# Performance work log

Hardware: AMD Instinct MI355X
Metric: run time of the kernel (lower is better)

## Reference

```python
import jax, jax.numpy as jnp
import numpy as np

N_INTT = 100000
N_MVTX = 100000
N_EDGES = 300000
IN_DIM = 64
OUT_DIM = 64
FEAT_DIM = 2 * OUT_DIM          # 128
EDGE_DIM = 2 * FEAT_DIM         # 256
H_DIM = IN_DIM + FEAT_DIM + 2 * EDGE_DIM  # 64+128+512 = 704


def _lin(key, fan_in, fan_out):
    k1, k2 = jax.random.split(key)
    bound = 1.0 / np.sqrt(fan_in)
    W = jax.random.uniform(k1, (fan_in, fan_out), jnp.float32, -bound, bound)
    b = jax.random.uniform(k2, (fan_out,), jnp.float32, -bound, bound)
    return W, b


def setup_inputs() -> dict:
    key = jax.random.key(0)
    ks = jax.random.split(key, 12)
    x_intt_0 = jax.random.normal(ks[0], (N_INTT, 3), jnp.float32)
    x_mvtx_0 = jax.random.normal(ks[1], (N_MVTX, 3), jnp.float32)
    x_intt = jax.random.normal(ks[2], (N_INTT, IN_DIM), jnp.float32)
    x_mvtx = jax.random.normal(ks[3], (N_MVTX, IN_DIM), jnp.float32)
    start = jax.random.randint(ks[4], (N_EDGES,), 0, N_INTT, jnp.int32)
    end = jax.random.randint(ks[5], (N_EDGES,), 0, N_MVTX, jnp.int32)
    edge_index = jnp.stack([start, end], axis=0)
    W_in_intt, b_in_intt = _lin(ks[6], IN_DIM, FEAT_DIM)
    W_in_mvtx, b_in_mvtx = _lin(ks[7], IN_DIM, FEAT_DIM)
    W_score, b_score = _lin(ks[8], EDGE_DIM, 1)
    W_out_intt, b_out_intt = _lin(ks[9], H_DIM, OUT_DIM)
    W_out_mvtx, b_out_mvtx = _lin(ks[10], H_DIM, OUT_DIM)
    return {
        "x_intt_0": x_intt_0, "x_mvtx_0": x_mvtx_0,
        "x_intt": x_intt, "x_mvtx": x_mvtx, "edge_index": edge_index,
        "W_in_intt": W_in_intt, "b_in_intt": b_in_intt,
        "W_in_mvtx": W_in_mvtx, "b_in_mvtx": b_in_mvtx,
        "W_score": W_score, "b_score": b_score,
        "W_out_intt": W_out_intt, "b_out_intt": b_out_intt,
        "W_out_mvtx": W_out_mvtx, "b_out_mvtx": b_out_mvtx,
    }


def _mean_max_pool(edges, idx, num_segments):
    # scatter_mean with zero-initialized out: mean over incident edges, 0 if none
    s = jax.ops.segment_sum(edges, idx, num_segments=num_segments)
    cnt = jax.ops.segment_sum(jnp.ones((edges.shape[0], 1), edges.dtype), idx,
                              num_segments=num_segments)
    mean = s / jnp.maximum(cnt, 1.0)
    # scatter_max with zero-initialized out: max includes the initial 0
    mx = jnp.maximum(jax.ops.segment_max(edges, idx, num_segments=num_segments), 0.0)
    return mean, mx


def reference(x_intt_0, x_mvtx_0, x_intt, x_mvtx, edge_index,
              W_in_intt, b_in_intt, W_in_mvtx, b_in_mvtx,
              W_score, b_score, W_out_intt, b_out_intt,
              W_out_mvtx, b_out_mvtx):
    # apply_constraints=False -> x_intt_0/x_mvtx_0 unused
    xp_intt = x_intt @ W_in_intt + b_in_intt        # [Ni, F]
    xp_mvtx = x_mvtx @ W_in_mvtx + b_in_mvtx        # [Nm, F]
    start, end = edge_index[0], edge_index[1]
    xp = jnp.concatenate([xp_intt[start], xp_mvtx[end]], axis=-1)  # [E, 2F]
    att = jnp.exp(-jnp.abs(xp @ W_score + b_score))  # potential activation, [E,1]
    edges = xp * att                                 # [E, 2F]
    mean_i, max_i = _mean_max_pool(edges, start, xp_intt.shape[0])
    mean_m, max_m = _mean_max_pool(edges, end, xp_mvtx.shape[0])
    H_intt = jnp.concatenate([x_intt, xp_intt, mean_i, max_i], axis=-1)  # [Ni, 704]
    H_mvtx = jnp.concatenate([x_mvtx, xp_mvtx, mean_m, max_m], axis=-1)
    h_intt = jax.nn.relu(H_intt @ W_out_intt + b_out_intt)
    h_mvtx = jax.nn.relu(H_mvtx @ W_out_mvtx + b_out_mvtx)
    return (h_intt, h_mvtx)
```

## Files before the change

### kernel.cpp

```cpp
#include <hip/hip_runtime.h>
#include <hip/hip_bf16.h>

typedef __hip_bfloat16 bf16;
typedef __attribute__((ext_vector_type(8))) short bf16x8;
typedef __attribute__((ext_vector_type(4))) float f32x4;

__device__ __forceinline__ float bfu(unsigned u) { return __uint_as_float(u << 16); }
__device__ __forceinline__ unsigned packbf(float a, float b) {
    return (unsigned)__bfloat16_as_ushort(__float2bfloat16(a)) |
           ((unsigned)__bfloat16_as_ushort(__float2bfloat16(b)) << 16);
}

#define CAP 32

#define NEL_O (704 * 64)

__global__ __launch_bounds__(256) void prep_kernel(
    const int* __restrict__ e_start, const int* __restrict__ e_end,
    int* __restrict__ deg_i, int* __restrict__ deg_m,
    int* __restrict__ list_i, int* __restrict__ list_m, int E, int fill_blocks,
    const float* __restrict__ Woi, const float* __restrict__ Wom,
    bf16* __restrict__ Wtoi, bf16* __restrict__ Wtom,
    const float* __restrict__ Wii, const float* __restrict__ Wim, int wt_blocks,
    const float* __restrict__ x_i, const float* __restrict__ b_i,
    const float* __restrict__ x_m, const float* __restrict__ b_m,
    const float* __restrict__ Wsc,
    bf16* __restrict__ xp_i, bf16* __restrict__ xp_m,
    float* __restrict__ sc_i, float* __restrict__ sc_m,
    int Ni, int Nm, int lin_bi)
{
    int bid = blockIdx.x;
    if (bid < fill_blocks) {
        int i = bid * 256 + threadIdx.x;
        if (i >= E) return;
        int s = e_start[i], e = e_end[i];
        int pi = atomicAdd(&deg_i[s], 1);
        if (pi < CAP) list_i[(size_t)s * CAP + pi] = e;
        int pm = atomicAdd(&deg_m[e], 1);
        if (pm < CAP) list_m[(size_t)e * CAP + pm] = s;
        return;
    }
    bid -= fill_blocks;
    if (bid < wt_blocks) {
        int tid = bid * 256 + threadIdx.x;
        if (tid >= 2 * NEL_O) return;
        int half = tid >= NEL_O;
        int t = tid - half * NEL_O;
        int j = t / 704, k = t % 704;
        const float* W = half ? Wom : Woi;
        bf16* Wt = half ? Wtom : Wtoi;
        Wt[(size_t)j * 704 + k] = __float2bfloat16(W[(size_t)k * 64 + j]);
        return;
    }
    bid -= wt_blocks;
    int side = bid >= lin_bi;
    int blk = side ? bid - lin_bi : bid;
    const float* x   = side ? x_m : x_i;
    const float* Win = side ? Wim : Wii;
    const float* b   = side ? b_m : b_i;
    const float* wsc = side ? Wsc + 128 : Wsc;
    bf16* xp = side ? xp_m : xp_i;
    float* sc = side ? sc_m : sc_i;
    int N = side ? Nm : Ni;

    int tid = threadIdx.x, wv = tid >> 6, lane = tid & 63;
    int frow = lane & 15, kg = lane >> 4;
    int n0 = blk * 64 + wv * 16;
    if (n0 >= N) return;
    int nrow = min(n0 + frow, N - 1);
    f32x4 acc[8];
#pragma unroll
    for (int nt = 0; nt < 8; ++nt) acc[nt] = (f32x4){0.f, 0.f, 0.f, 0.f};
#pragma unroll
    for (int kk = 0; kk < 2; ++kk) {
        const float* ap = x + (size_t)nrow * 64 + kk * 32 + kg * 8;
        float4 a0 = *(const float4*)ap;
        float4 a1 = *(const float4*)(ap + 4);
        union { unsigned u[4]; bf16x8 v; } au;
        au.u[0] = packbf(a0.x, a0.y); au.u[1] = packbf(a0.z, a0.w);
        au.u[2] = packbf(a1.x, a1.y); au.u[3] = packbf(a1.z, a1.w);
#pragma unroll
        for (int nt = 0; nt < 8; ++nt) {
            int col = nt * 16 + frow;
            const float* wp = Win + (size_t)(kk * 32 + kg * 8) * 128 + col;
            union { unsigned u[4]; bf16x8 v; } bu;
#pragma unroll
            for (int z = 0; z < 4; ++z)
                bu.u[z] = packbf(wp[(2 * z) * 128], wp[(2 * z + 1) * 128]);
            acc[nt] = __builtin_amdgcn_mfma_f32_16x16x32_bf16(au.v, bu.v, acc[nt], 0, 0, 0);
        }
    }
    float contrib[4] = {0.f, 0.f, 0.f, 0.f};
#pragma unroll
    for (int nt = 0; nt < 8; ++nt) {
        int col = nt * 16 + frow;
        float bj = b[col];
        float wj = wsc[col];
#pragma unroll
        for (int reg = 0; reg < 4; ++reg) {
            float v = acc[nt][reg] + bj;
            int n = n0 + kg * 4 + reg;
            if (n < N) xp[(size_t)n * 128 + col] = __float2bfloat16(v);
            contrib[reg] += v * wj;
        }
    }
#pragma unroll
    for (int off = 1; off < 16; off <<= 1) {
#pragma unroll
        for (int reg = 0; reg < 4; ++reg)
            contrib[reg] += __shfl_xor(contrib[reg], off, 64);
    }
    if (frow == 0) {
#pragma unroll
        for (int reg = 0; reg < 4; ++reg) {
            int n = n0 + kg * 4 + reg;
            if (n < N) sc[n] = contrib[reg];
        }
    }
}

#define BN 16
#define HS 716
__device__ __forceinline__ void accum8(uint4 g, float att, float* s, float* m) {
    unsigned gg[4] = {g.x, g.y, g.z, g.w};
#pragma unroll
    for (int k = 0; k < 4; ++k) {
        float t0 = att * bfu(gg[k] & 0xffffu);
        float t1 = att * bfu(gg[k] >> 16);
        s[2 * k] += t0;  s[2 * k + 1] += t1;
        m[2 * k] = fmaxf(m[2 * k], t0);  m[2 * k + 1] = fmaxf(m[2 * k + 1], t1);
    }
}

__global__ __launch_bounds__(256) void node_kernel(
    const float* __restrict__ x_i, const bf16* __restrict__ xp_i,
    const bf16* __restrict__ xp_m,
    const float* __restrict__ sc_i, const float* __restrict__ sc_m,
    const int* __restrict__ deg_i, const int* __restrict__ list_i,
    const bf16* __restrict__ Wt_oi, const float* __restrict__ b_oi,
    const float* __restrict__ x_m,
    const int* __restrict__ deg_m, const int* __restrict__ list_m,
    const bf16* __restrict__ Wt_om, const float* __restrict__ b_om,
    const float* __restrict__ bsc, float* __restrict__ out,
    int Ni, int Nm, int blocks_i)
{
    __shared__ bf16 Hs[BN][HS];
    int side = (int)blockIdx.x >= blocks_i;
    int blk = side ? blockIdx.x - blocks_i : blockIdx.x;
    const float* x        = side ? x_m : x_i;
    const bf16* xp_self   = side ? xp_m : xp_i;
    const bf16* xp_other  = side ? xp_i : xp_m;
    const float* sc_self  = side ? sc_m : sc_i;
    const float* sc_other = side ? sc_i : sc_m;
    const int* deg  = side ? deg_m : deg_i;
    const int* list = side ? list_m : list_i;
    const bf16* Wt  = side ? Wt_om : Wt_oi;
    const float* b  = side ? b_om : b_oi;
    float* outp = side ? out + (size_t)Ni * 64 : out;
    int N = side ? Nm : Ni;
    int self_first = side ? 0 : 1;

    int tid = threadIdx.x, wv = tid >> 6, lane = tid & 63;
    int ql = lane & 15, q4 = lane & 48;
    int r = wv * 4 + (lane >> 4);
    int n0 = blk * BN;
    int n = min(n0 + r, N - 1);

    float bias = bsc[0];
    int dg = deg[n];
    int dgc = min(dg, CAP);
    float ps = sc_self[n] + bias;
    uint4 us4 = *(const uint4*)(xp_self + (size_t)n * 128 + ql * 8);
    float4 xv4 = *(const float4*)(x + (size_t)n * 64 + ql * 4);

    int oa = 0, ob = 0;
    float sa = 0.f, sb = 0.f;
    if (ql < dgc)      oa = list[(size_t)n * CAP + ql];
    if (16 + ql < dgc) ob = list[(size_t)n * CAP + 16 + ql];
    if (ql < dgc)      sa = sc_other[oa];
    if (16 + ql < dgc) sb = sc_other[ob];
    float att_a = (ql < dgc)      ? __expf(-fabsf(ps + sa)) : 0.f;
    float att_b = (16 + ql < dgc) ? __expf(-fabsf(ps + sb)) : 0.f;

    float A = att_a + att_b;
    float Am = fmaxf(att_a, att_b);
#pragma unroll
    for (int off = 1; off < 16; off <<= 1) {
        A += __shfl_xor(A, off, 64);
        Am = fmaxf(Am, __shfl_xor(Am, off, 64));
    }

    float s[8], m[8];
#pragma unroll
    for (int k = 0; k < 8; ++k) { s[k] = 0.f; m[k] = 0.f; }

    int dmaxw = dgc;
    dmaxw = max(dmaxw, __shfl_xor(dmaxw, 16, 64));
    dmaxw = max(dmaxw, __shfl_xor(dmaxw, 32, 64));

    int dm0 = min(dmaxw, 16);
    for (int d = 0; d < dm0; d += 4) {
        uint4 g[4];
        float a[4];
#pragma unroll
        for (int j = 0; j < 4; ++j) {
            int dd = min(d + j, 15);
            bool p = (d + j < dgc);
            int o = __shfl(oa, q4 + dd, 64);
            a[j] = p ? __shfl(att_a, q4 + dd, 64) : 0.f;
            g[j] = (uint4){0u, 0u, 0u, 0u};
            if (p) g[j] = *(const uint4*)(xp_other + (size_t)o * 128 + ql * 8);
        }
#pragma unroll
        for (int j = 0; j < 4; ++j) accum8(g[j], a[j], s, m);
    }
    for (int d = 16; d < dmaxw; d += 2) {
#pragma unroll
        for (int j = 0; j < 2; ++j) {
            int dd = min(d + j - 16, 15);
            bool p = (d + j < dgc);
            int o = __shfl(ob, q4 + dd, 64);
            float a0 = p ? __shfl(att_b, q4 + dd, 64) : 0.f;
            uint4 g0 = (uint4){0u, 0u, 0u, 0u};
            if (p) g0 = *(const uint4*)(xp_other + (size_t)o * 128 + ql * 8);
            accum8(g0, a0, s, m);
        }
    }

    float inv = 1.0f / fmaxf((float)dg, 1.0f);
    float sA = A * inv, sAm = Am;
    int cm_self  = self_first ? 192 : 320;
    int cm_cross = self_first ? 320 : 192;
    int cx_self  = self_first ? 448 : 576;
    int cx_cross = self_first ? 576 : 448;
    char* row = (char*)&Hs[r][0];
    *(uint2*)(row + ql * 8) = make_uint2(packbf(xv4.x, xv4.y), packbf(xv4.z, xv4.w));
    *(uint4*)(row + 128 + ql * 16) = us4;
    unsigned uu[4] = {us4.x, us4.y, us4.z, us4.w};
    float xs[8];
#pragma unroll
    for (int k = 0; k < 4; ++k) {
        xs[2 * k] = bfu(uu[k] & 0xffffu);
        xs[2 * k + 1] = bfu(uu[k] >> 16);
    }
    uint4 wms, wxs, wmc, wxc;
    wms.x = packbf(xs[0] * sA, xs[1] * sA);  wms.y = packbf(xs[2] * sA, xs[3] * sA);
    wms.z = packbf(xs[4] * sA, xs[5] * sA);  wms.w = packbf(xs[6] * sA, xs[7] * sA);
    wxs.x = packbf(fmaxf(xs[0], 0.f) * sAm, fmaxf(xs[1], 0.f) * sAm);
    wxs.y = packbf(fmaxf(xs[2], 0.f) * sAm, fmaxf(xs[3], 0.f) * sAm);
    wxs.z = packbf(fmaxf(xs[4], 0.f) * sAm, fmaxf(xs[5], 0.f) * sAm);
    wxs.w = packbf(fmaxf(xs[6], 0.f) * sAm, fmaxf(xs[7], 0.f) * sAm);
    wmc.x = packbf(s[0] * inv, s[1] * inv);  wmc.y = packbf(s[2] * inv, s[3] * inv);
    wmc.z = packbf(s[4] * inv, s[5] * inv);  wmc.w = packbf(s[6] * inv, s[7] * inv);
    wxc.x = packbf(m[0], m[1]);  wxc.y = packbf(m[2], m[3]);
    wxc.z = packbf(m[4], m[5]);  wxc.w = packbf(m[6], m[7]);
    *(uint4*)(row + cm_self * 2 + ql * 16)  = wms;
    *(uint4*)(row + cx_self * 2 + ql * 16)  = wxs;
    *(uint4*)(row + cm_cross * 2 + ql * 16) = wmc;
    *(uint4*)(row + cx_cross * 2 + ql * 16) = wxc;
    __syncthreads();

    int frow = lane & 15;
    int kg = lane >> 4;
    const char* abase = (const char*)&Hs[frow][0] + kg * 16;
    const char* bbase = (const char*)(Wt + (size_t)(wv * 16 + frow) * 704) + kg * 16;
    f32x4 acc = {0.f, 0.f, 0.f, 0.f};
#pragma unroll
    for (int kt = 0; kt < 22; ++kt) {
        bf16x8 a  = *(const bf16x8*)(abase + kt * 64);
        bf16x8 bf = *(const bf16x8*)(bbase + kt * 64);
        acc = __builtin_amdgcn_mfma_f32_16x16x32_bf16(a, bf, acc, 0, 0, 0);
    }
    int ccol = wv * 16 + frow;
    float bj = b[ccol];
#pragma unroll
    for (int reg = 0; reg < 4; ++reg) {
        int crow = kg * 4 + reg;
        int nn = n0 + crow;
        if (nn < N) outp[(size_t)nn * 64 + ccol] = fmaxf(acc[reg] + bj, 0.f);
    }
}

extern "C" void kernel_launch(void* const* d_in, const int* in_sizes, int n_in,
                              void* d_out, int out_size, void* d_ws, size_t ws_size,
                              hipStream_t stream) {
    const float* x_i    = (const float*)d_in[2];
    const float* x_m    = (const float*)d_in[3];
    const int*   eidx   = (const int*)d_in[4];
    const float* W_in_i = (const float*)d_in[5];
    const float* b_in_i = (const float*)d_in[6];
    const float* W_in_m = (const float*)d_in[7];
    const float* b_in_m = (const float*)d_in[8];
    const float* W_sc   = (const float*)d_in[9];
    const float* b_sc   = (const float*)d_in[10];
    const float* W_o_i  = (const float*)d_in[11];
    const float* b_o_i  = (const float*)d_in[12];
    const float* W_o_m  = (const float*)d_in[13];
    const float* b_o_m  = (const float*)d_in[14];

    int Ni = in_sizes[2] / 64;
    int Nm = in_sizes[3] / 64;
    int E  = in_sizes[4] / 2;
    const int* e_start = eidx;
    const int* e_end   = eidx + E;

    char* base = (char*)d_ws;
    bf16* xp_i  = (bf16*)base;  base += (size_t)Ni * 128 * sizeof(bf16);
    bf16* xp_m  = (bf16*)base;  base += (size_t)Nm * 128 * sizeof(bf16);
    float* sc_i = (float*)base; base += (size_t)Ni * sizeof(float);
    float* sc_m = (float*)base; base += (size_t)Nm * sizeof(float);
    int* list_i = (int*)base;   base += (size_t)Ni * CAP * sizeof(int);
    int* list_m = (int*)base;   base += (size_t)Nm * CAP * sizeof(int);
    int* deg_i  = (int*)base;   base += (size_t)Ni * sizeof(int);
    int* deg_m  = (int*)base;   base += (size_t)Nm * sizeof(int);
    bf16* Wt_oi = (bf16*)base;  base += (size_t)704 * 64 * sizeof(bf16);
    bf16* Wt_om = (bf16*)base;  base += (size_t)704 * 64 * sizeof(bf16);
    hipMemsetAsync(deg_i, 0, ((size_t)Ni + Nm) * sizeof(int), stream);

    int fill_blocks = (E + 255) / 256;
    int wt_blocks = (2 * NEL_O + 255) / 256;
    int lin_bi = (Ni + 63) / 64, lin_bm = (Nm + 63) / 64;
    prep_kernel<<<fill_blocks + wt_blocks + lin_bi + lin_bm, 256, 0, stream>>>(
        e_start, e_end, deg_i, deg_m, list_i, list_m, E, fill_blocks,
        W_o_i, W_o_m, Wt_oi, Wt_om, W_in_i, W_in_m, wt_blocks,
        x_i, b_in_i, x_m, b_in_m, W_sc,
        xp_i, xp_m, sc_i, sc_m, Ni, Nm, lin_bi);

    float* out = (float*)d_out;
    int nb_i = (Ni + BN - 1) / BN, nb_m = (Nm + BN - 1) / BN;
    node_kernel<<<nb_i + nb_m, 256, 0, stream>>>(
        x_i, xp_i, xp_m, sc_i, sc_m, deg_i, list_i, Wt_oi, b_o_i,
        x_m, deg_m, list_m, Wt_om, b_o_m, b_sc, out, Ni, Nm, nb_i);
}
```

Baseline: 221.7 us.

## Precompute edge attention in separate fill kernel and store bf16 copies of x

Moves adjacency-list construction into its own kernel that runs after the projection kernel. It computes each edge's attention weight once and stores it next to the neighbor index as a uint2 pair. The node kernel no longer gathers score values per neighbor or evaluates exp. Node features are also cached as bf16 during the projection stage so the node kernel reads half the bytes, and output stores are made nontemporal. In exchange it adds a kernel launch, serializes the fill step after the projection, and doubles the size of the adjacency lists.

Measured after the change: 230.7 us. 1.04x slower.

```diff
diff --git a/kernel.cpp b/kernel.cpp
--- a/kernel.cpp
+++ b/kernel.cpp
@@ -4,6 +4,7 @@
 typedef __hip_bfloat16 bf16;
 typedef __attribute__((ext_vector_type(8))) short bf16x8;
 typedef __attribute__((ext_vector_type(4))) float f32x4;
+typedef __attribute__((ext_vector_type(2))) unsigned u32x2;
 
 __device__ __forceinline__ float bfu(unsigned u) { return __uint_as_float(u << 16); }
 __device__ __forceinline__ unsigned packbf(float a, float b) {
@@ -12,13 +13,9 @@
 }
 
 #define CAP 32
-
 #define NEL_O (704 * 64)
 
 __global__ __launch_bounds__(256) void prep_kernel(
-    const int* __restrict__ e_start, const int* __restrict__ e_end,
-    int* __restrict__ deg_i, int* __restrict__ deg_m,
-    int* __restrict__ list_i, int* __restrict__ list_m, int E, int fill_blocks,
     const float* __restrict__ Woi, const float* __restrict__ Wom,
     bf16* __restrict__ Wtoi, bf16* __restrict__ Wtom,
     const float* __restrict__ Wii, const float* __restrict__ Wim, int wt_blocks,
@@ -26,21 +23,11 @@
     const float* __restrict__ x_m, const float* __restrict__ b_m,
     const float* __restrict__ Wsc,
     bf16* __restrict__ xp_i, bf16* __restrict__ xp_m,
+    bf16* __restrict__ xb_i, bf16* __restrict__ xb_m,
     float* __restrict__ sc_i, float* __restrict__ sc_m,
     int Ni, int Nm, int lin_bi)
 {
     int bid = blockIdx.x;
-    if (bid < fill_blocks) {
-        int i = bid * 256 + threadIdx.x;
-        if (i >= E) return;
-        int s = e_start[i], e = e_end[i];
-        int pi = atomicAdd(&deg_i[s], 1);
-        if (pi < CAP) list_i[(size_t)s * CAP + pi] = e;
-        int pm = atomicAdd(&deg_m[e], 1);
-        if (pm < CAP) list_m[(size_t)e * CAP + pm] = s;
-        return;
-    }
-    bid -= fill_blocks;
     if (bid < wt_blocks) {
         int tid = bid * 256 + threadIdx.x;
         if (tid >= 2 * NEL_O) return;
@@ -60,6 +47,7 @@
     const float* b   = side ? b_m : b_i;
     const float* wsc = side ? Wsc + 128 : Wsc;
     bf16* xp = side ? xp_m : xp_i;
+    bf16* xb = side ? xb_m : xb_i;
     float* sc = side ? sc_m : sc_i;
     int N = side ? Nm : Ni;
 
@@ -79,6 +67,7 @@
         union { unsigned u[4]; bf16x8 v; } au;
         au.u[0] = packbf(a0.x, a0.y); au.u[1] = packbf(a0.z, a0.w);
         au.u[2] = packbf(a1.x, a1.y); au.u[3] = packbf(a1.z, a1.w);
+        *(bf16x8*)(xb + (size_t)nrow * 64 + kk * 32 + kg * 8) = au.v;
 #pragma unroll
         for (int nt = 0; nt < 8; ++nt) {
             int col = nt * 16 + frow;
@@ -119,6 +108,24 @@
     }
 }
 
+__global__ __launch_bounds__(256) void fill_kernel(
+    const int* __restrict__ e_start, const int* __restrict__ e_end,
+    const float* __restrict__ sc_i, const float* __restrict__ sc_m,
+    const float* __restrict__ bsc,
+    int* __restrict__ deg_i, int* __restrict__ deg_m,
+    uint2* __restrict__ list_i, uint2* __restrict__ list_m, int E)
+{
+    int i = blockIdx.x * 256 + threadIdx.x;
+    if (i >= E) return;
+    int s = e_start[i], e = e_end[i];
+    float att = __expf(-fabsf(sc_i[s] + sc_m[e] + bsc[0]));
+    unsigned au = __float_as_uint(att);
+    int pi = atomicAdd(&deg_i[s], 1);
+    if (pi < CAP) list_i[(size_t)s * CAP + pi] = make_uint2((unsigned)e, au);
+    int pm = atomicAdd(&deg_m[e], 1);
+    if (pm < CAP) list_m[(size_t)e * CAP + pm] = make_uint2((unsigned)s, au);
+}
+
 #define BN 16
 #define HS 716
 __device__ __forceinline__ void accum8(uint4 g, float att, float* s, float* m) {
@@ -133,27 +140,23 @@
 }
 
 __global__ __launch_bounds__(256) void node_kernel(
-    const float* __restrict__ x_i, const bf16* __restrict__ xp_i,
+    const bf16* __restrict__ xb_i, const bf16* __restrict__ xp_i,
     const bf16* __restrict__ xp_m,
-    const float* __restrict__ sc_i, const float* __restrict__ sc_m,
-    const int* __restrict__ deg_i, const int* __restrict__ list_i,
+    const int* __restrict__ deg_i, const uint2* __restrict__ list_i,
     const bf16* __restrict__ Wt_oi, const float* __restrict__ b_oi,
-    const float* __restrict__ x_m,
-    const int* __restrict__ deg_m, const int* __restrict__ list_m,
+    const bf16* __restrict__ xb_m,
+    const int* __restrict__ deg_m, const uint2* __restrict__ list_m,
     const bf16* __restrict__ Wt_om, const float* __restrict__ b_om,
-    const float* __restrict__ bsc, float* __restrict__ out,
-    int Ni, int Nm, int blocks_i)
+    float* __restrict__ out, int Ni, int Nm, int blocks_i)
 {
     __shared__ bf16 Hs[BN][HS];
     int side = (int)blockIdx.x >= blocks_i;
     int blk = side ? blockIdx.x - blocks_i : blockIdx.x;
-    const float* x        = side ? x_m : x_i;
+    const bf16* xb        = side ? xb_m : xb_i;
     const bf16* xp_self   = side ? xp_m : xp_i;
     const bf16* xp_other  = side ? xp_i : xp_m;
-    const float* sc_self  = side ? sc_m : sc_i;
-    const float* sc_other = side ? sc_i : sc_m;
     const int* deg  = side ? deg_m : deg_i;
-    const int* list = side ? list_m : list_i;
+    const uint2* list = side ? list_m : list_i;
     const bf16* Wt  = side ? Wt_om : Wt_oi;
     const float* b  = side ? b_om : b_oi;
     float* outp = side ? out + (size_t)Ni * 64 : out;
@@ -166,21 +169,16 @@
     int n0 = blk * BN;
     int n = min(n0 + r, N - 1);
 
-    float bias = bsc[0];
     int dg = deg[n];
     int dgc = min(dg, CAP);
-    float ps = sc_self[n] + bias;
     uint4 us4 = *(const uint4*)(xp_self + (size_t)n * 128 + ql * 8);
-    float4 xv4 = *(const float4*)(x + (size_t)n * 64 + ql * 4);
-
-    int oa = 0, ob = 0;
-    float sa = 0.f, sb = 0.f;
-    if (ql < dgc)      oa = list[(size_t)n * CAP + ql];
-    if (16 + ql < dgc) ob = list[(size_t)n * CAP + 16 + ql];
-    if (ql < dgc)      sa = sc_other[oa];
-    if (16 + ql < dgc) sb = sc_other[ob];
-    float att_a = (ql < dgc)      ? __expf(-fabsf(ps + sa)) : 0.f;
-    float att_b = (16 + ql < dgc) ? __expf(-fabsf(ps + sb)) : 0.f;
+    u32x2 xv = *(const u32x2*)(xb + (size_t)n * 64 + ql * 4);
+
+    int d16 = min(dgc, 16);
+    uint2 ea = (ql < d16)       ? list[(size_t)n * CAP + ql]      : make_uint2(0u, 0u);
+    uint2 eb = (16 + ql < dgc)  ? list[(size_t)n * CAP + 16 + ql] : make_uint2(0u, 0u);
+    int oa = (int)ea.x;  float att_a = __uint_as_float(ea.y);
+    int ob = (int)eb.x;  float att_b = __uint_as_float(eb.y);
 
     float A = att_a + att_b;
     float Am = fmaxf(att_a, att_b);
@@ -234,7 +232,7 @@
     int cx_self  = self_first ? 448 : 576;
     int cx_cross = self_first ? 576 : 448;
     char* row = (char*)&Hs[r][0];
-    *(uint2*)(row + ql * 8) = make_uint2(packbf(xv4.x, xv4.y), packbf(xv4.z, xv4.w));
+    *(uint2*)(row + ql * 8) = make_uint2(xv.x, xv.y);
     *(uint4*)(row + 128 + ql * 16) = us4;
     unsigned uu[4] = {us4.x, us4.y, us4.z, us4.w};
     float xs[8];
@@ -277,7 +275,9 @@
     for (int reg = 0; reg < 4; ++reg) {
         int crow = kg * 4 + reg;
         int nn = n0 + crow;
-        if (nn < N) outp[(size_t)nn * 64 + ccol] = fmaxf(acc[reg] + bj, 0.f);
+        if (nn < N)
+            __builtin_nontemporal_store(fmaxf(acc[reg] + bj, 0.f),
+                                        &outp[(size_t)nn * 64 + ccol]);
     }
 }
 
@@ -307,28 +307,31 @@
     char* base = (char*)d_ws;
     bf16* xp_i  = (bf16*)base;  base += (size_t)Ni * 128 * sizeof(bf16);
     bf16* xp_m  = (bf16*)base;  base += (size_t)Nm * 128 * sizeof(bf16);
+    bf16* xb_i  = (bf16*)base;  base += (size_t)Ni * 64 * sizeof(bf16);
+    bf16* xb_m  = (bf16*)base;  base += (size_t)Nm * 64 * sizeof(bf16);
     float* sc_i = (float*)base; base += (size_t)Ni * sizeof(float);
     float* sc_m = (float*)base; base += (size_t)Nm * sizeof(float);
-    int* list_i = (int*)base;   base += (size_t)Ni * CAP * sizeof(int);
-    int* list_m = (int*)base;   base += (size_t)Nm * CAP * sizeof(int);
+    uint2* list_i = (uint2*)base; base += (size_t)Ni * CAP * sizeof(uint2);
+    uint2* list_m = (uint2*)base; base += (size_t)Nm * CAP * sizeof(uint2);
+    bf16* Wt_oi = (bf16*)base;  base += (size_t)704 * 64 * sizeof(bf16);
+    bf16* Wt_om = (bf16*)base;  base += (size_t)704 * 64 * sizeof(bf16);
     int* deg_i  = (int*)base;   base += (size_t)Ni * sizeof(int);
     int* deg_m  = (int*)base;   base += (size_t)Nm * sizeof(int);
-    bf16* Wt_oi = (bf16*)base;  base += (size_t)704 * 64 * sizeof(bf16);
-    bf16* Wt_om = (bf16*)base;  base += (size_t)704 * 64 * sizeof(bf16);
     hipMemsetAsync(deg_i, 0, ((size_t)Ni + Nm) * sizeof(int), stream);
 
-    int fill_blocks = (E + 255) / 256;
     int wt_blocks = (2 * NEL_O + 255) / 256;
     int lin_bi = (Ni + 63) / 64, lin_bm = (Nm + 63) / 64;
-    prep_kernel<<<fill_blocks + wt_blocks + lin_bi + lin_bm, 256, 0, stream>>>(
-        e_start, e_end, deg_i, deg_m, list_i, list_m, E, fill_blocks,
+    prep_kernel<<<wt_blocks + lin_bi + lin_bm, 256, 0, stream>>>(
         W_o_i, W_o_m, Wt_oi, Wt_om, W_in_i, W_in_m, wt_blocks,
         x_i, b_in_i, x_m, b_in_m, W_sc,
-        xp_i, xp_m, sc_i, sc_m, Ni, Nm, lin_bi);
+        xp_i, xp_m, xb_i, xb_m, sc_i, sc_m, Ni, Nm, lin_bi);
+
+    fill_kernel<<<(E + 255) / 256, 256, 0, stream>>>(
+        e_start, e_end, sc_i, sc_m, b_sc, deg_i, deg_m, list_i, list_m, E);
 
     float* out = (float*)d_out;
     int nb_i = (Ni + BN - 1) / BN, nb_m = (Nm + BN - 1) / BN;
     node_kernel<<<nb_i + nb_m, 256, 0, stream>>>(
-        x_i, xp_i, xp_m, sc_i, sc_m, deg_i, list_i, Wt_oi, b_o_i,
-        x_m, deg_m, list_m, Wt_om, b_o_m, b_sc, out, Ni, Nm, nb_i);
-}
+        xb_i, xp_i, xp_m, deg_i, list_i, Wt_oi, b_o_i,
+        xb_m, deg_m, list_m, Wt_om, b_o_m, out, Ni, Nm, nb_i);
+}
```
